# Performance work log

Measured on AMD Instinct MI355X. Metric: run time of the kernel, lower is better.

Reference implementation:

```python
import jax, jax.numpy as jnp
import numpy as np

NUM_EMBEDDINGS = 1024
EMBEDDING_DIM = 256
COMMITMENT_COST = 0.25


def setup_inputs() -> dict:
    key = jax.random.key(0)
    k1, k2 = jax.random.split(key)
    inputs = jax.random.normal(k1, (32, EMBEDDING_DIM, 32, 32), dtype=jnp.float32)
    # torch init: uniform_(-1/K, 1/K)
    emb_w = jax.random.uniform(k2, (NUM_EMBEDDINGS, EMBEDDING_DIM), dtype=jnp.float32,
                               minval=-1.0 / NUM_EMBEDDINGS, maxval=1.0 / NUM_EMBEDDINGS)
    return {"inputs": inputs, "emb_w": emb_w}


def reference(inputs, emb_w):
    sg = jax.lax.stop_gradient
    # BCHW -> BHWC
    x = jnp.transpose(inputs, (0, 2, 3, 1))
    in_shape = x.shape
    flat = x.reshape(-1, EMBEDDING_DIM)  # [N, D]
    # squared L2 distances to codebook: [N, K]
    distances = (jnp.sum(flat * flat, axis=1, keepdims=True)
                 + jnp.sum(emb_w * emb_w, axis=1)
                 - 2.0 * jnp.matmul(flat, emb_w.T))
    idx = jnp.argmin(distances, axis=1)  # [N]
    encodings = jax.nn.one_hot(idx, NUM_EMBEDDINGS, dtype=jnp.float32)  # [N, K]
    # one-hot @ codebook == gather
    quantized = jnp.take(emb_w, idx, axis=0).reshape(in_shape)  # [B,H,W,D]
    e_latent_loss = jnp.mean((sg(quantized) - x) ** 2)
    q_latent_loss = jnp.mean((quantized - sg(x)) ** 2)
    loss = q_latent_loss + COMMITMENT_COST * e_latent_loss
    # straight-through estimator
    quantized_st = x + sg(quantized - x)
    avg_probs = jnp.mean(encodings, axis=0)
    perplexity = jnp.exp(-jnp.sum(avg_probs * jnp.log(avg_probs + 1e-10)))
    return (loss, jnp.transpose(quantized_st, (0, 3, 1, 2)), perplexity, encodings)
```

## Files before the change

### kernel.cpp

```cpp
#include <hip/hip_runtime.h>
#include <hip/hip_bf16.h>

typedef short short8 __attribute__((ext_vector_type(8)));
typedef float f32x4 __attribute__((ext_vector_type(4)));
typedef unsigned short u16x4 __attribute__((ext_vector_type(4)));

#define D_ 256
#define K_ 1024
#define HW_ 1024
#define NROWS_ 32768
#define QELEMS 8388608
#define NBLK_ (NROWS_ / 64)

static __device__ __forceinline__ unsigned short to_bf16(float v) {
    __hip_bfloat16 h = __float2bfloat16(v);
    return *(unsigned short*)&h;
}

__global__ __launch_bounds__(256) void vq_prep(const float* __restrict__ emb,
    unsigned short* __restrict__ ebf2, float* __restrict__ enorm,
    int* __restrict__ counts, double* __restrict__ loss_acc)
{
    __shared__ float part[256];
    const int ct = blockIdx.x, t = threadIdx.x;
    const int col = t & 15, s = t >> 4;
    const int k = ct * 16 + col;
    const f32x4* src = (const f32x4*)(emb + (size_t)k * D_ + s * 16);
    short8 f0, f1;
    float a = 0.f;
#pragma unroll
    for (int j = 0; j < 4; ++j) {
        f32x4 v = src[j];
#pragma unroll
        for (int q = 0; q < 4; ++q) {
            int idx = j * 4 + q;
            unsigned short h = to_bf16(v[q]);
            a = fmaf(v[q], v[q], a);
            if (idx < 8) f0[idx] = (short)h; else f1[idx - 8] = (short)h;
        }
    }
    part[t] = a;
    char* base = (char*)ebf2 + ct * 8192 + (s >> 1) * 1024 + ((s & 1) * 2) * 256 + col * 16;
    *(short8*)base = f0;
    *(short8*)(base + 256) = f1;
    __syncthreads();
    if (t < 16) {
        float s2 = 0.f;
#pragma unroll
        for (int j = 0; j < 16; ++j) s2 += part[t + 16 * j];
        enorm[ct * 16 + t] = s2;
    }
    if (ct < 4) counts[ct * 256 + t] = 0;
    if (ct == 0 && t == 0) *loss_acc = 0.0;
}

__global__ __launch_bounds__(512, 4) void vq_main(
    const float* __restrict__ x, const float* __restrict__ emb,
    const unsigned short* __restrict__ ebf2, const float* __restrict__ enorm,
    int* __restrict__ counts, double* __restrict__ loss_acc, float* __restrict__ out)
{
    __shared__ char smem[65536];
    __shared__ float xn[64][9];
    __shared__ float rminv[64][4];
    __shared__ int   rmini[64][4];
    __shared__ int   bestsh[64];

    char* xs = smem;

    const int t = threadIdx.x;
    const int n0 = blockIdx.x * 64;
    const int b = n0 >> 10;
    const int hw0 = n0 & 1023;
    const float* xbase = x + (size_t)b * (D_ * HW_) + hw0;

    {
        const int rt = t & 15, r0 = rt * 4;
        const int dg = t >> 4;
        float xp[4] = {0.f, 0.f, 0.f, 0.f};
#pragma unroll
        for (int m = 0; m < 2; ++m) {
            int d0 = (dg + 32 * m) * 4;
            f32x4 c[4];
#pragma unroll
            for (int q = 0; q < 4; ++q)
                c[q] = *(const f32x4*)(xbase + (size_t)(d0 + q) * HW_ + r0);
            const int dc = d0 >> 5, kg = (d0 >> 3) & 3, off = (d0 & 7) * 2;
#pragma unroll
            for (int i = 0; i < 4; ++i) {
                u16x4 pk;
                pk[0] = to_bf16(c[0][i]); pk[1] = to_bf16(c[1][i]);
                pk[2] = to_bf16(c[2][i]); pk[3] = to_bf16(c[3][i]);
                xp[i] = fmaf(c[0][i], c[0][i], xp[i]);
                xp[i] = fmaf(c[1][i], c[1][i], xp[i]);
                xp[i] = fmaf(c[2][i], c[2][i], xp[i]);
                xp[i] = fmaf(c[3][i], c[3][i], xp[i]);
                int r = r0 + i;
                int byte = ((r >> 4) << 13) + (dc << 10) + (kg << 8) + ((r & 15) << 4) + off;
                *(u16x4*)(xs + byte) = pk;
            }
        }
#pragma unroll
        for (int i = 0; i < 4; ++i) {
            xp[i] += __shfl_down(xp[i], 32);
            xp[i] += __shfl_down(xp[i], 16);
        }
        if ((t & 48) == 0) {
            int w0 = t >> 6;
#pragma unroll
            for (int i = 0; i < 4; ++i) xn[r0 + i][w0] = xp[i];
        }
    }

    const int lane = t & 63;
    const int w = t >> 6;
    const int rh = w & 1;
    const int cq = w >> 1;
    const int col = lane & 15;
    const char* eb = (const char*)ebf2;

    __syncthreads();

    short8 areg[2][8];
#pragma unroll
    for (int rt = 0; rt < 2; ++rt) {
        const char* ab = xs + ((rh * 2 + rt) << 13);
#pragma unroll
        for (int dc = 0; dc < 8; ++dc)
            areg[rt][dc] = *(const short8*)(ab + dc * 1024 + lane * 16);
    }

    float v1[8]; int i1[8];
#pragma unroll
    for (int s = 0; s < 8; ++s) { v1[s] = 3.4e38f; i1[s] = 0x7fffffff; }

    float2* ezw = (float2*)(out + 8388610 + (size_t)(n0 + w * 8) * 1024);
    const float2 zz = {0.f, 0.f};

    for (int cc = 0; cc < 16; ++cc) {
        const char* tb = eb + cc * 32768 + (cq << 13);
        short8 bf[8];
#pragma unroll
        for (int dc = 0; dc < 8; ++dc)
            bf[dc] = *(const short8*)(tb + dc * 1024 + lane * 16);
        f32x4 acc0 = {0.f, 0.f, 0.f, 0.f};
        f32x4 acc1 = {0.f, 0.f, 0.f, 0.f};
#pragma unroll
        for (int dc = 0; dc < 8; ++dc) {
            acc0 = __builtin_amdgcn_mfma_f32_16x16x32_bf16(areg[0][dc], bf[dc], acc0, 0, 0, 0);
            acc1 = __builtin_amdgcn_mfma_f32_16x16x32_bf16(areg[1][dc], bf[dc], acc1, 0, 0, 0);
        }
        const int code = cc * 64 + cq * 16 + col;
        const float bn = enorm[code];
#pragma unroll
        for (int r = 0; r < 4; ++r) {
            float dv = fmaf(-2.f, acc0[r], bn);
            if (dv < v1[r]) { v1[r] = dv; i1[r] = code; }
            float dw = fmaf(-2.f, acc1[r], bn);
            if (dw < v1[4 + r]) { v1[4 + r] = dw; i1[4 + r] = code; }
        }
        float2* ez = ezw + cc * 256;
#pragma unroll
        for (int j = 0; j < 4; ++j) ez[j * 64 + lane] = zz;
    }

#pragma unroll
    for (int mask = 1; mask < 16; mask <<= 1) {
#pragma unroll
        for (int s = 0; s < 8; ++s) {
            float ov = __shfl_xor(v1[s], mask);
            int oi = __shfl_xor(i1[s], mask);
            if (ov < v1[s] || (ov == v1[s] && oi < i1[s])) { v1[s] = ov; i1[s] = oi; }
        }
    }
    {
        const int kg = lane >> 4;
        if (col == 0) {
#pragma unroll
            for (int s = 0; s < 8; ++s) {
                int rt = s >> 2, r = s & 3;
                int row = rh * 32 + rt * 16 + kg * 4 + r;
                rminv[row][cq] = v1[s];
                rmini[row][cq] = i1[s];
            }
        }
    }
    __syncthreads();

    if (t < 64) {
        float dmin = rminv[t][0]; int best = rmini[t][0];
#pragma unroll
        for (int g = 1; g < 4; ++g) {
            float cv = rminv[t][g]; int ci = rmini[t][g];
            if (cv < dmin || (cv == dmin && ci < best)) { dmin = cv; best = ci; }
        }
        bestsh[t] = best;
        atomicAdd(&counts[best], 1);
        float s = 0.f;
#pragma unroll
        for (int g = 0; g < 8; ++g) s += xn[t][g];
        float lrow = dmin + s;
        for (int o = 32; o > 0; o >>= 1) lrow += __shfl_down(lrow, o);
        if (t == 0) atomicAdd(loss_acc, (double)lrow);
    }
    __syncthreads();

    {
        int r = w * 8 + (lane >> 3);
        int c = lane & 7;
        const f32x4* src4 = (const f32x4*)emb + (size_t)bestsh[r] * 64;
        float* q = (float*)smem + r * 256;
        int xr = r & 31;
#pragma unroll
        for (int j = 0; j < 8; ++j) {
            f32x4 v = src4[8 * j + c];
#pragma unroll
            for (int kq = 0; kq < 4; ++kq) {
                int d = 4 * (8 * j + c) + kq;
                q[d ^ xr] = v[kq];
            }
        }
    }
    __syncthreads();

    {
        const int hwr = t & 63;
        const int dq = t >> 6;
        float* outq = out + 1 + (size_t)b * (D_ * HW_) + hw0 + hwr;
        const float* q = (const float*)smem + hwr * 256;
        int xr = hwr & 31;
#pragma unroll
        for (int dd = 0; dd < 32; ++dd) {
            int d = dq + dd * 8;
            outq[(size_t)d * HW_] = q[d ^ xr];
        }
    }
    if (t < 64) out[8388610 + (size_t)(n0 + t) * 1024 + bestsh[t]] = 1.0f;
}

__global__ __launch_bounds__(256) void vq_fin(const int* __restrict__ counts,
    const double* __restrict__ loss_acc, float* __restrict__ d_out)
{
    int t = threadIdx.x;
    double s = 0.0;
    for (int k = t; k < K_; k += 256) {
        double p = (double)counts[k] / 32768.0;
        s += p * log(p + 1e-10);
    }
    for (int o = 32; o > 0; o >>= 1) s += __shfl_down(s, o);
    __shared__ double sred[4];
    if ((t & 63) == 0) sred[t >> 6] = s;
    __syncthreads();
    if (t == 0) {
        double tot = sred[0] + sred[1] + sred[2] + sred[3];
        d_out[0] = (float)(1.25 * (*loss_acc) / (double)QELEMS);
        d_out[8388609] = (float)exp(-tot);
    }
}

extern "C" void kernel_launch(void* const* d_in, const int* in_sizes, int n_in,
                              void* d_out, int out_size, void* d_ws, size_t ws_size,
                              hipStream_t stream)
{
    const float* x = (const float*)d_in[0];
    const float* emb = (const float*)d_in[1];
    char* ws = (char*)d_ws;
    unsigned short* ebf2 = (unsigned short*)(ws);
    float* enorm = (float*)(ws + 524288);
    int* counts = (int*)(ws + 528384);
    double* lacc = (double*)(ws + 532480);
    float* out = (float*)d_out;

    vq_prep<<<64, 256, 0, stream>>>(emb, ebf2, enorm, counts, lacc);
    vq_main<<<NBLK_, 512, 0, stream>>>(x, emb, ebf2, enorm, counts, lacc, out);
    vq_fin<<<1, 256, 0, stream>>>(counts, lacc, out);
}
```

Measured before the change: 62.44 us.

## Halve rows per block to 32 with 256-thread blocks for more blocks

The main VQ kernel now handles 32 input rows per block with 4 waves instead of 64 rows with 8 waves, which doubles the grid to 1024 blocks and halves the LDS footprint. The row-to-wave mapping, the norm reductions and the epilogue indexing are reworked to match. The intent is better load balance and occupancy across CUs, and more blocks in flight to hide memory latency. In exchange, each codebook tile from global/L2 is reused by only half as many rows, so codebook traffic doubles.

Result: slower. 66.46 us (+6.4%).

```diff
diff --git a/kernel.cpp b/kernel.cpp
--- a/kernel.cpp
+++ b/kernel.cpp
@@ -3,6 +3,7 @@
 
 typedef short short8 __attribute__((ext_vector_type(8)));
 typedef float f32x4 __attribute__((ext_vector_type(4)));
+typedef float f32x2 __attribute__((ext_vector_type(2)));
 typedef unsigned short u16x4 __attribute__((ext_vector_type(4)));
 
 #define D_ 256
@@ -10,7 +11,7 @@
 #define HW_ 1024
 #define NROWS_ 32768
 #define QELEMS 8388608
-#define NBLK_ (NROWS_ / 64)
+#define NBLK_ (NROWS_ / 32)
 
 static __device__ __forceinline__ unsigned short to_bf16(float v) {
     __hip_bfloat16 h = __float2bfloat16(v);
@@ -54,28 +55,31 @@
     if (ct == 0 && t == 0) *loss_acc = 0.0;
 }
 
-__global__ __launch_bounds__(512, 4) void vq_main(
+__global__ __launch_bounds__(256, 4) void vq_main(
     const float* __restrict__ x, const float* __restrict__ emb,
     const unsigned short* __restrict__ ebf2, const float* __restrict__ enorm,
     int* __restrict__ counts, double* __restrict__ loss_acc, float* __restrict__ out)
 {
-    __shared__ char smem[65536];
-    __shared__ float xn[64][9];
-    __shared__ float rminv[64][4];
-    __shared__ int   rmini[64][4];
-    __shared__ int   bestsh[64];
+    __shared__ char smem[32768];
+    __shared__ float xn[32][4];
+    __shared__ float rminv[32][4];
+    __shared__ int   rmini[32][4];
+    __shared__ int   bestsh[32];
 
     char* xs = smem;
 
     const int t = threadIdx.x;
-    const int n0 = blockIdx.x * 64;
+    const int n0 = blockIdx.x * 32;
     const int b = n0 >> 10;
     const int hw0 = n0 & 1023;
     const float* xbase = x + (size_t)b * (D_ * HW_) + hw0;
 
-    {
-        const int rt = t & 15, r0 = rt * 4;
-        const int dg = t >> 4;
+    const int lane = t & 63;
+    const int w = t >> 6;
+
+    {
+        const int rt = t & 7, r0 = rt * 4;
+        const int dg = t >> 3;
         float xp[4] = {0.f, 0.f, 0.f, 0.f};
 #pragma unroll
         for (int m = 0; m < 2; ++m) {
@@ -103,18 +107,15 @@
         for (int i = 0; i < 4; ++i) {
             xp[i] += __shfl_down(xp[i], 32);
             xp[i] += __shfl_down(xp[i], 16);
-        }
-        if ((t & 48) == 0) {
-            int w0 = t >> 6;
-#pragma unroll
-            for (int i = 0; i < 4; ++i) xn[r0 + i][w0] = xp[i];
-        }
-    }
-
-    const int lane = t & 63;
-    const int w = t >> 6;
-    const int rh = w & 1;
-    const int cq = w >> 1;
+            xp[i] += __shfl_down(xp[i], 8);
+        }
+        if ((lane & 56) == 0) {
+#pragma unroll
+            for (int i = 0; i < 4; ++i) xn[r0 + i][w] = xp[i];
+        }
+    }
+
+    const int cq = w;
     const int col = lane & 15;
     const char* eb = (const char*)ebf2;
 
@@ -123,7 +124,7 @@
     short8 areg[2][8];
 #pragma unroll
     for (int rt = 0; rt < 2; ++rt) {
-        const char* ab = xs + ((rh * 2 + rt) << 13);
+        const char* ab = xs + (rt << 13);
 #pragma unroll
         for (int dc = 0; dc < 8; ++dc)
             areg[rt][dc] = *(const short8*)(ab + dc * 1024 + lane * 16);
@@ -133,8 +134,8 @@
 #pragma unroll
     for (int s = 0; s < 8; ++s) { v1[s] = 3.4e38f; i1[s] = 0x7fffffff; }
 
-    float2* ezw = (float2*)(out + 8388610 + (size_t)(n0 + w * 8) * 1024);
-    const float2 zz = {0.f, 0.f};
+    f32x2* ezw = (f32x2*)(out + 8388610 + (size_t)(n0 + w * 8) * 1024);
+    const f32x2 zz = {0.f, 0.f};
 
     for (int cc = 0; cc < 16; ++cc) {
         const char* tb = eb + cc * 32768 + (cq << 13);
@@ -158,7 +159,7 @@
             float dw = fmaf(-2.f, acc1[r], bn);
             if (dw < v1[4 + r]) { v1[4 + r] = dw; i1[4 + r] = code; }
         }
-        float2* ez = ezw + cc * 256;
+        f32x2* ez = ezw + cc * 256;
 #pragma unroll
         for (int j = 0; j < 4; ++j) ez[j * 64 + lane] = zz;
     }
@@ -178,7 +179,7 @@
 #pragma unroll
             for (int s = 0; s < 8; ++s) {
                 int rt = s >> 2, r = s & 3;
-                int row = rh * 32 + rt * 16 + kg * 4 + r;
+                int row = rt * 16 + kg * 4 + r;
                 rminv[row][cq] = v1[s];
                 rmini[row][cq] = i1[s];
             }
@@ -186,7 +187,7 @@
     }
     __syncthreads();
 
-    if (t < 64) {
+    if (t < 32) {
         float dmin = rminv[t][0]; int best = rmini[t][0];
 #pragma unroll
         for (int g = 1; g < 4; ++g) {
@@ -195,46 +196,42 @@
         }
         bestsh[t] = best;
         atomicAdd(&counts[best], 1);
-        float s = 0.f;
-#pragma unroll
-        for (int g = 0; g < 8; ++g) s += xn[t][g];
+        float s = xn[t][0] + xn[t][1] + xn[t][2] + xn[t][3];
         float lrow = dmin + s;
-        for (int o = 32; o > 0; o >>= 1) lrow += __shfl_down(lrow, o);
+        for (int o = 16; o > 0; o >>= 1) lrow += __shfl_down(lrow, o);
         if (t == 0) atomicAdd(loss_acc, (double)lrow);
     }
     __syncthreads();
 
     {
-        int r = w * 8 + (lane >> 3);
-        int c = lane & 7;
+        int r = t >> 3;
+        int c = t & 7;
         const f32x4* src4 = (const f32x4*)emb + (size_t)bestsh[r] * 64;
         float* q = (float*)smem + r * 256;
-        int xr = r & 31;
 #pragma unroll
         for (int j = 0; j < 8; ++j) {
             f32x4 v = src4[8 * j + c];
 #pragma unroll
             for (int kq = 0; kq < 4; ++kq) {
                 int d = 4 * (8 * j + c) + kq;
-                q[d ^ xr] = v[kq];
+                q[d ^ r] = v[kq];
             }
         }
     }
     __syncthreads();
 
     {
-        const int hwr = t & 63;
-        const int dq = t >> 6;
+        const int hwr = t & 31;
+        const int dq = t >> 5;
         float* outq = out + 1 + (size_t)b * (D_ * HW_) + hw0 + hwr;
         const float* q = (const float*)smem + hwr * 256;
-        int xr = hwr & 31;
 #pragma unroll
         for (int dd = 0; dd < 32; ++dd) {
             int d = dq + dd * 8;
-            outq[(size_t)d * HW_] = q[d ^ xr];
-        }
-    }
-    if (t < 64) out[8388610 + (size_t)(n0 + t) * 1024 + bestsh[t]] = 1.0f;
+            outq[(size_t)d * HW_] = q[d ^ hwr];
+        }
+    }
+    if (t < 32) out[8388610 + (size_t)(n0 + t) * 1024 + bestsh[t]] = 1.0f;
 }
 
 __global__ __launch_bounds__(256) void vq_fin(const int* __restrict__ counts,
@@ -271,6 +268,6 @@
     float* out = (float*)d_out;
 
     vq_prep<<<64, 256, 0, stream>>>(emb, ebf2, enorm, counts, lacc);
-    vq_main<<<NBLK_, 512, 0, stream>>>(x, emb, ebf2, enorm, counts, lacc, out);
+    vq_main<<<NBLK_, 256, 0, stream>>>(x, emb, ebf2, enorm, counts, lacc, out);
     vq_fin<<<1, 256, 0, stream>>>(counts, lacc, out);
 }
```
